# Optimization experiments

Measured on AMD Instinct MI355X. Metric: run time of the kernel, lower is better.

Reference implementation:

```python
import jax, jax.numpy as jnp
import numpy as np

B, S, D = 4, 1024, 1024
H, DK, DH = 16, 64, 64  # num_heads, key_size, head_size
NEG = 1e12


def setup_inputs() -> dict:
    key = jax.random.key(0)
    ks = jax.random.split(key, 16)
    scale = 0.02
    inp = {
        'q': jax.random.normal(ks[0], (B, S, D), jnp.float32),
        'k': jax.random.normal(ks[1], (B, S, D), jnp.float32),
        'v': jax.random.normal(ks[2], (B, S, D), jnp.float32),
        'v_mask': jax.random.randint(ks[3], (B, S), 0, 2, jnp.int32),
        'q_mask': jax.random.randint(ks[4], (B, S), 0, 2, jnp.int32),
        # causal attention mask (float, 1 = keep)
        'a_mask': jnp.tril(jnp.ones((S, S), jnp.float32))[None, None, :, :],
        'Wq': jax.random.normal(ks[5], (D, H * DK), jnp.float32) * scale,
        'bq': jnp.zeros((H * DK,), jnp.float32),
        'Wk': jax.random.normal(ks[6], (D, H * DK), jnp.float32) * scale,
        'bk': jnp.zeros((H * DK,), jnp.float32),
        'Wv': jax.random.normal(ks[7], (D, H * DH), jnp.float32) * scale,
        'bv': jnp.zeros((H * DH,), jnp.float32),
        'Wo': jax.random.normal(ks[8], (H * DH, H * DH), jnp.float32) * scale,
        'bo': jnp.zeros((H * DH,), jnp.float32),
    }
    return inp


def reference(q, k, v, v_mask, q_mask, a_mask, Wq, bq, Wk, bk, Wv, bv, Wo, bo):
    b, sq, _ = q.shape
    sk = k.shape[1]
    qw = (jnp.einsum('bsd,de->bse', q, Wq) + bq).reshape(b, sq, H, DK)
    kw = (jnp.einsum('bsd,de->bse', k, Wk) + bk).reshape(b, sk, H, DK)
    vw = (jnp.einsum('bsd,de->bse', v, Wv) + bv).reshape(b, sk, H, DH)
    # scores [b, h, sq, sk]
    a = jnp.einsum('bjhd,bkhd->bhjk', qw, kw) / jnp.sqrt(jnp.float32(DK))
    vm = v_mask.astype(jnp.float32)  # [b, sk]
    a = a - (1.0 - vm)[:, None, None, :] * NEG  # sequence_masking mode='add'
    a = a - (1.0 - a_mask) * NEG                # attention mask
    p = jax.nn.softmax(a, axis=-1)
    o = jnp.einsum('bhjk,bkhd->bjhd', p, vw).reshape(b, sq, H * DH)
    o = jnp.einsum('bse,ef->bsf', o, Wo) + bo
    qm = q_mask.astype(jnp.float32)
    o = o * qm[:, :, None]  # sequence_masking mode='mul'
    return o
```

## Files before the change

kernel.cpp:

```cpp
#include <hip/hip_runtime.h>
#include <cstdint>
#include <cstddef>

typedef unsigned short u16;
using short8 = __attribute__((ext_vector_type(8))) short;
using f32x4  = __attribute__((ext_vector_type(4))) float;

constexpr int Sc = 1024;
constexpr float PEN = 60.0f;

__device__ __forceinline__ u16 f2bf(float f) {
  union { float f; uint32_t u; } v; v.f = f;
  return (u16)((v.u + 0x7fffu + ((v.u >> 16) & 1u)) >> 16);
}

__device__ __forceinline__ void gload_lds16(const u16* g, u16* l) {
  __builtin_amdgcn_global_load_lds(
      (const __attribute__((address_space(1))) uint32_t*)g,
      (__attribute__((address_space(3))) uint32_t*)l, 16, 0, 0);
}

__device__ __forceinline__ f32x4 mfma16(short8 a, short8 b, f32x4 c) {
  return __builtin_amdgcn_mfma_f32_16x16x32_bf16(a, b, c, 0, 0, 0);
}

__global__ __launch_bounds__(256) void prep(
    const float* __restrict__ q, const float* __restrict__ k,
    const float* __restrict__ v, u16* __restrict__ qb, u16* __restrict__ kb,
    u16* __restrict__ vb, const float* __restrict__ W0,
    const float* __restrict__ W1, const float* __restrict__ W2,
    const float* __restrict__ W3, u16* __restrict__ D0, u16* __restrict__ D1,
    u16* __restrict__ D2, u16* __restrict__ D3) {
  const int y = blockIdx.y;
  if (y < 3) {
    const float* src = y == 0 ? q : y == 1 ? k : v;
    u16* dst = y == 0 ? qb : y == 1 ? kb : vb;
    int i = blockIdx.x * 256 + threadIdx.x;
    float4 a = ((const float4*)src)[2 * i];
    float4 b = ((const float4*)src)[2 * i + 1];
    u16 t[8] = {f2bf(a.x), f2bf(a.y), f2bf(a.z), f2bf(a.w),
                f2bf(b.x), f2bf(b.y), f2bf(b.z), f2bf(b.w)};
    ((uint4*)dst)[i] = *(const uint4*)t;
  } else {
    if (blockIdx.x >= 1024) return;
    const int z = y - 3;
    const float* W = z == 0 ? W0 : z == 1 ? W1 : z == 2 ? W2 : W3;
    u16* WT = z == 0 ? D0 : z == 1 ? D1 : z == 2 ? D2 : D3;
    __shared__ float t[32][33];
    int bx = (blockIdx.x & 31) * 32, by = (blockIdx.x >> 5) * 32;
    int tx = threadIdx.x & 31, ty = threadIdx.x >> 5;
    for (int i = 0; i < 32; i += 8)
      t[ty + i][tx] = W[(size_t)(by + ty + i) * 1024 + bx + tx];
    __syncthreads();
    for (int i = 0; i < 32; i += 8)
      WT[(size_t)(bx + ty + i) * 1024 + by + tx] = f2bf(t[tx][ty + i]);
  }
}

__global__ __launch_bounds__(256, 6) void gemm_qkv(
    const u16* __restrict__ qb, const u16* __restrict__ kb,
    const u16* __restrict__ vb, const u16* __restrict__ BT,
    const float* __restrict__ bq, const float* __restrict__ bk,
    const float* __restrict__ bv, u16* __restrict__ QW, u16* __restrict__ KW,
    u16* __restrict__ VTg) {
  const int bid = blockIdx.x;
  const int xcd = bid & 7, local = bid >> 3;
  const int mp = local & 3, nbi = local >> 2;
  const int m0 = (xcd * 4 + mp) * 128, n0 = nbi * 64;
  const int seg = nbi >> 4;
  const u16* A    = seg == 0 ? qb : seg == 1 ? kb : vb;
  const float* bias = seg == 0 ? bq : seg == 1 ? bk : bv;

  __shared__ u16 As0[128 * 32], As1[128 * 32];
  __shared__ u16 Bs0[64 * 32], Bs1[64 * 32];

  const int t = threadIdx.x, w = t >> 6, lane = t & 63;
  const int q4 = lane >> 4, lm = lane & 15;
  const int wm = (w >> 1) * 64, wn = (w & 1) * 32;
  const int srow = lane >> 2, p = lane & 3;
  const int cf = q4 ^ ((lm >> 2) & 3);

  const int rbA0 = (w * 2) * 16, rbA1 = (w * 2 + 1) * 16, rbB = w * 16;
  const int rowA0 = rbA0 + srow, rowA1 = rbA1 + srow, rowB = rbB + srow;
  const int cA0 = p ^ ((rowA0 >> 2) & 3), cA1 = p ^ ((rowA1 >> 2) & 3);
  const int cB = p ^ ((rowB >> 2) & 3);
  const u16* pa0 = &A[(size_t)(m0 + rowA0) * 1024 + cA0 * 8];
  const u16* pa1 = &A[(size_t)(m0 + rowA1) * 1024 + cA1 * 8];
  const u16* pb  = &BT[(size_t)(n0 + rowB) * 1024 + cB * 8];

  f32x4 acc[4][2] = {};

  auto stage = [&](u16* as, u16* bs) {
    gload_lds16(pa0, as + rbA0 * 32);
    gload_lds16(pa1, as + rbA1 * 32);
    gload_lds16(pb, bs + rbB * 32);
    pa0 += 32; pa1 += 32; pb += 32;
  };
  auto compute = [&](const u16* as, const u16* bs) {
    short8 af[4], bf[2];
    for (int mi = 0; mi < 4; ++mi)
      af[mi] = *(const short8*)&as[(wm + mi * 16 + lm) * 32 + cf * 8];
    for (int ni = 0; ni < 2; ++ni)
      bf[ni] = *(const short8*)&bs[(wn + ni * 16 + lm) * 32 + cf * 8];
    for (int mi = 0; mi < 4; ++mi)
      for (int ni = 0; ni < 2; ++ni)
        acc[mi][ni] = mfma16(af[mi], bf[ni], acc[mi][ni]);
  };

  stage(As0, Bs0);
  for (int it = 0; it < 16; ++it) {
    __syncthreads();
    stage(As1, Bs1);
    compute(As0, Bs0);
    __syncthreads();
    if (it < 15) stage(As0, Bs0);
    compute(As1, Bs1);
  }

  if (seg < 2) {
    u16* C = seg == 0 ? QW : KW;
    for (int mi = 0; mi < 4; ++mi)
      for (int ni = 0; ni < 2; ++ni)
        for (int r = 0; r < 4; ++r) {
          int row = m0 + wm + mi * 16 + q4 * 4 + r;
          int col = (n0 + wn + ni * 16 + lm) & 1023;
          C[(size_t)row * 1024 + col] = f2bf(acc[mi][ni][r] + bias[col]);
        }
  } else {
    for (int mi = 0; mi < 4; ++mi)
      for (int ni = 0; ni < 2; ++ni) {
        int row0 = m0 + wm + mi * 16 + q4 * 4;
        int col = (n0 + wn + ni * 16 + lm) & 1023;
        float bv4 = bias[col];
        u16 o4[4];
        for (int r = 0; r < 4; ++r) o4[r] = f2bf(acc[mi][ni][r] + bv4);
        *(uint2*)&VTg[(size_t)col * 4096 + row0] = *(const uint2*)o4;
      }
  }
}

__global__ __launch_bounds__(256, 4) void gemm_out(
    const u16* __restrict__ A, const u16* __restrict__ BT,
    const float* __restrict__ bias, const int* __restrict__ qmask,
    float* __restrict__ Cf) {
  const int bid = blockIdx.x;
  const int xcd = bid & 7, local = bid >> 3;
  const int mp = local & 7, nb = local >> 3;
  const int m0 = (xcd * 8 + mp) * 64, n0 = nb * 64;

  __shared__ u16 As0[64 * 32], As1[64 * 32];
  __shared__ u16 Bs0[64 * 32], Bs1[64 * 32];
  const int t = threadIdx.x, w = t >> 6, lane = t & 63;
  const int q4 = lane >> 4, lm = lane & 15;
  const int wm = (w >> 1) * 32, wn = (w & 1) * 32;
  const int srow = lane >> 2, p = lane & 3;
  const int cf = q4 ^ ((lm >> 2) & 3);

  const int rb = w * 16;
  const int rowS = rb + srow;
  const int cS = p ^ ((rowS >> 2) & 3);
  const u16* pa = &A[(size_t)(m0 + rowS) * 1024 + cS * 8];
  const u16* pb = &BT[(size_t)(n0 + rowS) * 1024 + cS * 8];

  f32x4 acc[2][2] = {};

  auto stage = [&](u16* as, u16* bs) {
    gload_lds16(pa, as + rb * 32);
    gload_lds16(pb, bs + rb * 32);
    pa += 32; pb += 32;
  };
  auto compute = [&](const u16* as, const u16* bs) {
    short8 af[2], bf[2];
    for (int mi = 0; mi < 2; ++mi)
      af[mi] = *(const short8*)&as[(wm + mi * 16 + lm) * 32 + cf * 8];
    for (int ni = 0; ni < 2; ++ni)
      bf[ni] = *(const short8*)&bs[(wn + ni * 16 + lm) * 32 + cf * 8];
    for (int mi = 0; mi < 2; ++mi)
      for (int ni = 0; ni < 2; ++ni)
        acc[mi][ni] = mfma16(af[mi], bf[ni], acc[mi][ni]);
  };

  stage(As0, Bs0);
  for (int it = 0; it < 16; ++it) {
    __syncthreads();
    stage(As1, Bs1);
    compute(As0, Bs0);
    __syncthreads();
    if (it < 15) stage(As0, Bs0);
    compute(As1, Bs1);
  }

  for (int mi = 0; mi < 2; ++mi)
    for (int ni = 0; ni < 2; ++ni)
      for (int r = 0; r < 4; ++r) {
        int row = m0 + wm + mi * 16 + q4 * 4 + r;
        int col = n0 + wn + ni * 16 + lm;
        Cf[(size_t)row * 1024 + col] =
            (acc[mi][ni][r] + bias[col]) * (float)qmask[row];
      }
}

__global__ __launch_bounds__(64, 3) void attn(
    const u16* __restrict__ QW, const u16* __restrict__ KW,
    const u16* __restrict__ VTg, const int* __restrict__ vmask,
    u16* __restrict__ O) {
  const int bid = blockIdx.x;
  const int X = bid >> 8;
  const int rA = (bid >> 6) & 3, rB = 3 - rA;
  const int bh = bid & 63;
  const int b = bh >> 4, h = bh & 15;
  const int lane = threadIdx.x;
  const int q4 = lane >> 4, lm = lane & 15;

  const int qtA = X, qtB = 15 - X;
  const int TA = 2 * qtA + (rA >> 1), TB = 2 * qtB + (rB >> 1);
  const int RA = qtA * 64 + rA * 16, RB = qtB * 64 + rB * 16;

  __shared__ u16 Ks[2][32 * 64];
  __shared__ u16 P[16 * 40];
  __shared__ unsigned char penb[1024];

  {
    const int4* vmp = (const int4*)(vmask + b * 1024);
    for (int j = 0; j < 4; ++j) {
      int4 vm = vmp[4 * lane + j];
      unsigned char m4[4] = {
          (unsigned char)(vm.x == 0), (unsigned char)(vm.y == 0),
          (unsigned char)(vm.z == 0), (unsigned char)(vm.w == 0)};
      *(unsigned int*)&penb[16 * lane + 4 * j] = *(const unsigned int*)m4;
    }
  }
  int anyA = 0, anyB = 0;
  for (int i = lane; i <= qtB * 64; i += 64) {
    int un = (penb[i] == 0);
    if (i <= qtA * 64) anyA |= un;
    anyB |= un;
  }
  const int extA = (__ballot(anyA) == 0);
  const int extB = (__ballot(anyB) == 0);
  const int kend = (extA || extB) ? 31 : TB;

  short8 qfA[2], qfB[2];
  auto loadQ = [&](int R, short8 (&qf)[2]) {
    const u16* qp = &QW[(size_t)(b * Sc + R + lm) * 1024 + h * 64];
    qf[0] = *(const short8*)&qp[q4 * 8];
    qf[1] = *(const short8*)&qp[32 + q4 * 8];
    for (int fi = 0; fi < 2; ++fi)
      for (int i = 0; i < 8; ++i) {
        u16 x = (u16)qf[fi][i];
        int e = (x >> 7) & 0xff;
        qf[fi][i] = (short)(e > 3 ? (u16)(x - 0x180) : (u16)(x & 0x8000));
      }
  };
  loadQ(RA, qfA);
  loadQ(RB, qfB);

  float lA[4] = {}, lB[4] = {};
  f32x4 oaccA[4] = {}, oaccB[4] = {};
  const int qr0A = RA + q4 * 4, qr0B = RB + q4 * 4;

  const u16* Kbase = &KW[(size_t)(b * Sc) * 1024 + h * 64];
  const u16* Vbase = &VTg[(size_t)(h * 64) * 4096 + b * Sc];

  const int r0 = lane >> 3, pos = lane & 7, ch = pos ^ r0;
  auto stageK = [&](int kt, int buf) {
    for (int j = 0; j < 4; ++j) {
      int row = j * 8 + r0;
      gload_lds16(Kbase + (size_t)(kt * 32 + row) * 1024 + ch * 8,
                  &Ks[buf][j * 512]);
    }
  };

  auto strip = [&](const short8 (&qf)[2], f32x4 (&oacc)[4], float (&lr)[4],
                   int Tdiag, int qr0, int kt, int buf, const short8 (&vf)[4]) {
    const int mode = kt > Tdiag ? 2 : (kt == Tdiag ? 1 : 0);
    f32x4 sacc[2] = {};
    __builtin_amdgcn_s_setprio(1);
#pragma unroll
    for (int ni = 0; ni < 2; ++ni) {
      int row = ni * 16 + lm;
      short8 kf0 = *(const short8*)&Ks[buf][row * 64 + ((q4 ^ (lm & 7)) * 8)];
      short8 kf1 = *(const short8*)&Ks[buf][row * 64 + (((4 + q4) ^ (lm & 7)) * 8)];
      sacc[ni] = mfma16(qf[0], kf0, sacc[ni]);
      sacc[ni] = mfma16(qf[1], kf1, sacc[ni]);
    }
    __builtin_amdgcn_s_setprio(0);

#pragma unroll
    for (int ni = 0; ni < 2; ++ni) {
      int key = kt * 32 + ni * 16 + lm;
      float pen = penb[key] ? PEN : 0.0f;
      if (mode == 2) pen += PEN;
#pragma unroll
      for (int r = 0; r < 4; ++r) {
        float x = sacc[ni][r] - pen;
        if (mode == 1 && key > qr0 + r) x -= PEN;
        float pv = __expf(x);
        lr[r] += pv;
        P[(q4 * 4 + r) * 40 + ni * 16 + lm] = f2bf(pv);
      }
    }
    short8 pf = *(const short8*)&P[lm * 40 + q4 * 8];
    __builtin_amdgcn_s_setprio(1);
#pragma unroll
    for (int ni = 0; ni < 4; ++ni)
      oacc[ni] = mfma16(pf, vf[ni], oacc[ni]);
    __builtin_amdgcn_s_setprio(0);
  };

  stageK(0, 0);
  for (int kt = 0; kt <= kend; ++kt) {
    const int buf = kt & 1;
    short8 vf[4];
#pragma unroll
    for (int ni = 0; ni < 4; ++ni)
      vf[ni] = *(const short8*)(Vbase + (size_t)(ni * 16 + lm) * 4096 +
                                kt * 32 + q4 * 8);
    if (kt < kend) {
      stageK(kt + 1, buf ^ 1);
      asm volatile("s_waitcnt vmcnt(8)" ::: "memory");
    } else {
      asm volatile("s_waitcnt vmcnt(4)" ::: "memory");
    }
    __builtin_amdgcn_sched_barrier(0);

    if (kt <= TA) strip(qfA, oaccA, lA, TA, qr0A, kt, buf, vf);
    else if (extA) strip(qfA, oaccA, lA, TA, qr0A, kt, buf, vf);
    if (kt <= TB) strip(qfB, oaccB, lB, TB, qr0B, kt, buf, vf);
    else if (extB) strip(qfB, oaccB, lB, TB, qr0B, kt, buf, vf);
  }

  auto epilogue = [&](f32x4 (&oacc)[4], float (&lr)[4], int qr0) {
    for (int r = 0; r < 4; ++r) {
      float l = lr[r];
      for (int off = 1; off < 16; off <<= 1) l += __shfl_xor(l, off, 64);
      lr[r] = 1.0f / l;
    }
    for (int ni = 0; ni < 4; ++ni)
      for (int r = 0; r < 4; ++r) {
        int row = b * Sc + qr0 + r;
        O[(size_t)row * 1024 + h * 64 + ni * 16 + lm] =
            f2bf(oacc[ni][r] * lr[r]);
      }
  };
  epilogue(oaccA, lA, qr0A);
  epilogue(oaccB, lB, qr0B);
}

extern "C" void kernel_launch(void* const* d_in, const int* in_sizes, int n_in,
                              void* d_out, int out_size, void* d_ws, size_t ws_size,
                              hipStream_t stream) {
  (void)in_sizes; (void)n_in; (void)out_size; (void)ws_size;
  const float* q  = (const float*)d_in[0];
  const float* k  = (const float*)d_in[1];
  const float* v  = (const float*)d_in[2];
  const int* vmask = (const int*)d_in[3];
  const int* qmask = (const int*)d_in[4];
  const float* Wq = (const float*)d_in[6];
  const float* bq = (const float*)d_in[7];
  const float* Wk = (const float*)d_in[8];
  const float* bk = (const float*)d_in[9];
  const float* Wv = (const float*)d_in[10];
  const float* bv = (const float*)d_in[11];
  const float* Wo = (const float*)d_in[12];
  const float* bo = (const float*)d_in[13];

  char* ws = (char*)d_ws;
  u16* WT3 = (u16*)ws;
  u16* WoT = (u16*)(ws + 6291456);
  u16* QW  = (u16*)(ws + 8388608);
  u16* KW  = (u16*)(ws + 16777216);
  u16* VTg = (u16*)(ws + 25165824);
  u16* Oat = (u16*)(ws + 33554432);
  u16* qb = (u16*)d_out;
  u16* kb = (u16*)d_out + 4194304;
  u16* vb = Oat;

  dim3 tb(256);
  prep<<<dim3(2048, 7), tb, 0, stream>>>(q, k, v, qb, kb, vb, Wq, Wk, Wv, Wo,
                                         WT3, WT3 + 1048576, WT3 + 2097152,
                                         WoT);
  gemm_qkv<<<dim3(1536), tb, 0, stream>>>(qb, kb, vb, WT3, bq, bk, bv, QW, KW,
                                          VTg);
  attn<<<dim3(2048), dim3(64), 0, stream>>>(QW, KW, VTg, vmask, Oat);
  gemm_out<<<dim3(1024), tb, 0, stream>>>(Oat, WoT, bo, qmask, (float*)d_out);
}
```

Before: 229.4 us.

## Compute transposed scores so P feeds PV MFMA from registers, skipping LDS

```diff
diff --git a/kernel.cpp b/kernel.cpp
--- a/kernel.cpp
+++ b/kernel.cpp
@@ -217,22 +217,23 @@
   const int RA = qtA * 64 + rA * 16, RB = qtB * 64 + rB * 16;
 
   __shared__ u16 Ks[2][32 * 64];
-  __shared__ u16 P[16 * 40];
-  __shared__ unsigned char penb[1024];
+  __shared__ float penf[1024];
 
   {
     const int4* vmp = (const int4*)(vmask + b * 1024);
     for (int j = 0; j < 4; ++j) {
       int4 vm = vmp[4 * lane + j];
-      unsigned char m4[4] = {
-          (unsigned char)(vm.x == 0), (unsigned char)(vm.y == 0),
-          (unsigned char)(vm.z == 0), (unsigned char)(vm.w == 0)};
-      *(unsigned int*)&penb[16 * lane + 4 * j] = *(const unsigned int*)m4;
+      float4 p4;
+      p4.x = (1.f - (float)vm.x) * PEN;
+      p4.y = (1.f - (float)vm.y) * PEN;
+      p4.z = (1.f - (float)vm.z) * PEN;
+      p4.w = (1.f - (float)vm.w) * PEN;
+      *(float4*)&penf[16 * lane + 4 * j] = p4;
     }
   }
   int anyA = 0, anyB = 0;
   for (int i = lane; i <= qtB * 64; i += 64) {
-    int un = (penb[i] == 0);
+    int un = (penf[i] == 0.f);
     if (i <= qtA * 64) anyA |= un;
     anyB |= un;
   }
@@ -255,9 +256,9 @@
   loadQ(RA, qfA);
   loadQ(RB, qfB);
 
-  float lA[4] = {}, lB[4] = {};
+  float lsA = 0.f, lsB = 0.f;
   f32x4 oaccA[4] = {}, oaccB[4] = {};
-  const int qr0A = RA + q4 * 4, qr0B = RB + q4 * 4;
+  const int qrowA = RA + lm, qrowB = RB + lm;
 
   const u16* Kbase = &KW[(size_t)(b * Sc) * 1024 + h * 64];
   const u16* Vbase = &VTg[(size_t)(h * 64) * 4096 + b * Sc];
@@ -265,14 +266,15 @@
   const int r0 = lane >> 3, pos = lane & 7, ch = pos ^ r0;
   auto stageK = [&](int kt, int buf) {
     for (int j = 0; j < 4; ++j) {
-      int row = j * 8 + r0;
-      gload_lds16(Kbase + (size_t)(kt * 32 + row) * 1024 + ch * 8,
+      int lrow = j * 8 + r0;
+      int key = 2 * (lrow & 15) + (lrow >> 4);
+      gload_lds16(Kbase + (size_t)(kt * 32 + key) * 1024 + ch * 8,
                   &Ks[buf][j * 512]);
     }
   };
 
-  auto strip = [&](const short8 (&qf)[2], f32x4 (&oacc)[4], float (&lr)[4],
-                   int Tdiag, int qr0, int kt, int buf, const short8 (&vf)[4]) {
+  auto strip = [&](const short8 (&qf)[2], f32x4 (&oacc)[4], float& lsum,
+                   int Tdiag, int qrow, int kt, int buf, const short8 (&vf)[4]) {
     const int mode = kt > Tdiag ? 2 : (kt == Tdiag ? 1 : 0);
     f32x4 sacc[2] = {};
     __builtin_amdgcn_s_setprio(1);
@@ -281,30 +283,41 @@
       int row = ni * 16 + lm;
       short8 kf0 = *(const short8*)&Ks[buf][row * 64 + ((q4 ^ (lm & 7)) * 8)];
       short8 kf1 = *(const short8*)&Ks[buf][row * 64 + (((4 + q4) ^ (lm & 7)) * 8)];
-      sacc[ni] = mfma16(qf[0], kf0, sacc[ni]);
-      sacc[ni] = mfma16(qf[1], kf1, sacc[ni]);
+      sacc[ni] = mfma16(kf0, qf[0], sacc[ni]);
+      sacc[ni] = mfma16(kf1, qf[1], sacc[ni]);
     }
     __builtin_amdgcn_s_setprio(0);
 
-#pragma unroll
-    for (int ni = 0; ni < 2; ++ni) {
-      int key = kt * 32 + ni * 16 + lm;
-      float pen = penb[key] ? PEN : 0.0f;
-      if (mode == 2) pen += PEN;
+    f32x4 pna = *(const f32x4*)&penf[kt * 32 + 8 * q4];
+    f32x4 pnb = *(const f32x4*)&penf[kt * 32 + 8 * q4 + 4];
+    float pv[2][4];
+#pragma unroll
+    for (int ni = 0; ni < 2; ++ni)
 #pragma unroll
       for (int r = 0; r < 4; ++r) {
+        const int j = 2 * r + ni;
+        float pen = j < 4 ? pna[j] : pnb[j - 4];
         float x = sacc[ni][r] - pen;
-        if (mode == 1 && key > qr0 + r) x -= PEN;
-        float pv = __expf(x);
-        lr[r] += pv;
-        P[(q4 * 4 + r) * 40 + ni * 16 + lm] = f2bf(pv);
+        if (mode == 2) x -= PEN;
+        else if (mode == 1) {
+          int key = kt * 32 + 8 * q4 + j;
+          if (key > qrow) x -= PEN;
+        }
+        float e = __expf(x);
+        lsum += e;
+        pv[ni][r] = e;
       }
-    }
-    short8 pf = *(const short8*)&P[lm * 40 + q4 * 8];
+    uint32_t W0, W1, W2, W3;
+    asm("v_cvt_pk_bf16_f32 %0, %1, %2" : "=v"(W0) : "v"(pv[0][0]), "v"(pv[1][0]));
+    asm("v_cvt_pk_bf16_f32 %0, %1, %2" : "=v"(W1) : "v"(pv[0][1]), "v"(pv[1][1]));
+    asm("v_cvt_pk_bf16_f32 %0, %1, %2" : "=v"(W2) : "v"(pv[0][2]), "v"(pv[1][2]));
+    asm("v_cvt_pk_bf16_f32 %0, %1, %2" : "=v"(W3) : "v"(pv[0][3]), "v"(pv[1][3]));
+    union { uint32_t u[4]; short8 s; } pk;
+    pk.u[0] = W0; pk.u[1] = W1; pk.u[2] = W2; pk.u[3] = W3;
     __builtin_amdgcn_s_setprio(1);
 #pragma unroll
     for (int ni = 0; ni < 4; ++ni)
-      oacc[ni] = mfma16(pf, vf[ni], oacc[ni]);
+      oacc[ni] = mfma16(pk.s, vf[ni], oacc[ni]);
     __builtin_amdgcn_s_setprio(0);
   };
 
@@ -324,27 +337,33 @@
     }
     __builtin_amdgcn_sched_barrier(0);
 
-    if (kt <= TA) strip(qfA, oaccA, lA, TA, qr0A, kt, buf, vf);
-    else if (extA) strip(qfA, oaccA, lA, TA, qr0A, kt, buf, vf);
-    if (kt <= TB) strip(qfB, oaccB, lB, TB, qr0B, kt, buf, vf);
-    else if (extB) strip(qfB, oaccB, lB, TB, qr0B, kt, buf, vf);
-  }
-
-  auto epilogue = [&](f32x4 (&oacc)[4], float (&lr)[4], int qr0) {
+    if (kt <= TA) strip(qfA, oaccA, lsA, TA, qrowA, kt, buf, vf);
+    else if (extA) strip(qfA, oaccA, lsA, TA, qrowA, kt, buf, vf);
+    if (kt <= TB) strip(qfB, oaccB, lsB, TB, qrowB, kt, buf, vf);
+    else if (extB) strip(qfB, oaccB, lsB, TB, qrowB, kt, buf, vf);
+  }
+
+  auto epilogue = [&](f32x4 (&oacc)[4], float lsum, int Rbase) {
+    float l = lsum;
+    l += __shfl_xor(l, 16, 64);
+    l += __shfl_xor(l, 32, 64);
+    float linv[4];
+#pragma unroll
     for (int r = 0; r < 4; ++r) {
-      float l = lr[r];
-      for (int off = 1; off < 16; off <<= 1) l += __shfl_xor(l, off, 64);
-      lr[r] = 1.0f / l;
+      float lr = __shfl(l, (lane & 48) | (q4 * 4 + r), 64);
+      linv[r] = 1.0f / lr;
     }
+#pragma unroll
     for (int ni = 0; ni < 4; ++ni)
+#pragma unroll
       for (int r = 0; r < 4; ++r) {
-        int row = b * Sc + qr0 + r;
+        int row = b * Sc + Rbase + q4 * 4 + r;
         O[(size_t)row * 1024 + h * 64 + ni * 16 + lm] =
-            f2bf(oacc[ni][r] * lr[r]);
+            f2bf(oacc[ni][r] * linv[r]);
       }
   };
-  epilogue(oaccA, lA, qr0A);
-  epilogue(oaccB, lB, qr0B);
+  epilogue(oaccA, lsA, RA);
+  epilogue(oaccB, lsB, RB);
 }
 
 extern "C" void kernel_launch(void* const* d_in, const int* in_sizes, int n_in,
```

Measured after the change: 225.3 us. No clear change (-1.8%).
